# Kernel tuning notes

Measured on AMD Instinct MI355X. Metric: run time of the kernel, lower is better.

The kernel has to match this reference:

```python
import jax, jax.numpy as jnp
import numpy as np

N_NODES = 100000
N_EDGES = 1600000
D_NODE = 32
D_EDGE = 16
D_HID = 64
D_OUT = 32


def setup_inputs() -> dict:
    key = jax.random.key(0)
    ks = jax.random.split(key, 7)
    x = jax.random.normal(ks[0], (N_NODES, D_NODE), dtype=jnp.float32)
    edge_index = jax.random.randint(ks[1], (2, N_EDGES), 0, N_NODES, dtype=jnp.int64)
    edge_attr = jax.random.normal(ks[2], (N_EDGES, D_EDGE), dtype=jnp.float32)
    # 2-layer MLP params (Linear -> ReLU -> Linear), He-ish scaling
    W1 = jax.random.normal(ks[3], (D_NODE + D_EDGE, D_HID), dtype=jnp.float32) * (2.0 / (D_NODE + D_EDGE)) ** 0.5
    b1 = jnp.zeros((D_HID,), dtype=jnp.float32)
    W2 = jax.random.normal(ks[4], (D_HID, D_OUT), dtype=jnp.float32) * (2.0 / D_HID) ** 0.5
    b2 = jnp.zeros((D_OUT,), dtype=jnp.float32)
    return {"x": x, "edge_index": edge_index, "edge_attr": edge_attr,
            "W1": W1, "b1": b1, "W2": W2, "b2": b2}


def reference(x, edge_index, edge_attr, W1, b1, W2, b2):
    row, col = edge_index[0], edge_index[1]
    # gather source-node feats and concat with edge feats: [E, d_node + d_edge]
    inp = jnp.concatenate([x[col], edge_attr], axis=1)
    # 2-layer MLP over edges
    h = jax.nn.relu(inp @ W1 + b1)
    messages = h @ W2 + b2  # [E, d_out]
    # scatter-sum aggregate by destination node
    message = jax.ops.segment_sum(messages, row, num_segments=x.shape[0])
    return message
```

## Files before the change

kernel.cpp:

```cpp
#include <hip/hip_runtime.h>
#include <hip/hip_bf16.h>
#include <stdint.h>

#define N_NODES 100000
#define N_EDGES 1600000
#define D_NODE  32
#define D_EDGE  16
#define D_IN    48
#define D_HID   64
#define D_OUT   32

#define NBKT 98
#define BCAP 18432
#define SLICES (BCAP / 256)
#define S1_EDGES 2048
#define S1_NB 782
#define SCAN_NB 391

#define NFLAGS_OFF  ((size_t)0)
#define NB1_OFF     ((size_t)64)
#define NB2_OFF     ((size_t)320)
#define W1BF_OFF    ((size_t)1024)
#define W2BF_OFF    ((size_t)9216)
#define GCUR_OFF    ((size_t)16384)
#define XBF_OFF     ((size_t)65536)
#define TMPH_OFF    ((size_t)8388608)
#define TMPE_OFF    ((size_t)16777216)
#define REC_OFF     ((size_t)75497472)
#define ACCUM_OFF   ((size_t)90177536)

typedef __attribute__((ext_vector_type(8))) short bf16x8;
typedef __attribute__((ext_vector_type(4))) float f32x4;

__device__ inline float bf2f(unsigned int u16) {
    return __uint_as_float(u16 << 16);
}
__device__ inline unsigned short f2bf_rne(float f) {
    unsigned int x = __float_as_uint(f);
    unsigned int r = (x + 0x7FFFu + ((x >> 16) & 1u)) >> 16;
    return (unsigned short)r;
}
__device__ inline unsigned int pk_bf2(float a, float b) {
    float2 f; f.x = a; f.y = b;
    __hip_bfloat162 h = __float22bfloat162_rn(f);
    return *reinterpret_cast<unsigned int*>(&h);
}
__device__ inline float ld_f(const void* p, int i, int isbf) {
    if (isbf) return bf2f(((const unsigned short*)p)[i]);
    return ((const float*)p)[i];
}

__global__ __launch_bounds__(256) void prep_kernel(
        const void* __restrict__ xq, const void* __restrict__ idxq,
        const void* __restrict__ W1q, const void* __restrict__ b1q,
        const void* __restrict__ W2q, const void* __restrict__ b2q,
        char* __restrict__ ws) {
    const int t = threadIdx.x;
    const int i0 = blockIdx.x * 256 + t;

    __shared__ int s_isbf;
    if (t < 64) {
        unsigned short u = ((const unsigned short*)xq)[t];
        unsigned long long mb = __ballot(((u >> 7) & 0xFF) >= 140);
        if (t == 0) s_isbf = (mb == 0ULL);
    }

    float4* acc4 = (float4*)(ws + ACCUM_OFF);
    float4 z; z.x = z.y = z.z = z.w = 0.0f;
    for (int i = i0; i < (N_NODES + 1) * 32 / 4; i += SCAN_NB * 256) acc4[i] = z;

    __syncthreads();
    const int isbf = s_isbf;

    unsigned short* xbf = (unsigned short*)(ws + XBF_OFF);
    for (int i = i0; i < N_NODES * 32 / 8; i += SCAN_NB * 256) {
        uint4 o;
        if (isbf) {
            o = ((const uint4*)xq)[i];
        } else {
            const float4* xp = (const float4*)xq + i * 2;
            float4 a = xp[0], b = xp[1];
            o.x = pk_bf2(a.x, a.y); o.y = pk_bf2(a.z, a.w);
            o.z = pk_bf2(b.x, b.y); o.w = pk_bf2(b.z, b.w);
        }
        ((uint4*)xbf)[i] = o;
    }

    if (blockIdx.x != 0) return;

    if (t < NBKT) ((int*)(ws + GCUR_OFF))[t] = t * BCAP;
    if (t < 64) {
        int wodd = ((const int*)idxq)[2 * t + 1];
        unsigned long long mi = __ballot(wodd != 0);
        if (t == 0) {
            int* flags = (int*)(ws + NFLAGS_OFF);
            flags[0] = isbf;
            flags[1] = (mi == 0ULL);
        }
    }

    float* b1 = (float*)(ws + NB1_OFF);
    float* b2 = (float*)(ws + NB2_OFF);
    unsigned short* w1b = (unsigned short*)(ws + W1BF_OFF);
    unsigned short* w2b = (unsigned short*)(ws + W2BF_OFF);

    if (t < D_HID) b1[t] = ld_f(b1q, t, isbf);
    if (t < D_OUT) b2[t] = ld_f(b2q, t, isbf);

    for (int i = t; i < D_HID * 64; i += 256) {
        int n = i >> 6, k = i & 63;
        float v = (k < D_IN) ? ld_f(W1q, k * D_HID + n, isbf) : 0.0f;
        w1b[i] = f2bf_rne(v);
    }
    for (int i = t; i < D_OUT * 64; i += 256) {
        int n = i >> 6, k = i & 63;
        w2b[i] = f2bf_rne(ld_f(W2q, k * D_OUT + n, isbf));
    }
}

__global__ __launch_bounds__(256) void partition_kernel(
        const void* __restrict__ idxq, const void* __restrict__ eaq,
        char* __restrict__ ws) {
    const int is64 = ((const int*)(ws + NFLAGS_OFF))[1];
    const int isbf = ((const int*)(ws + NFLAGS_OFF))[0];
    __shared__ int hist[NBKT];
    __shared__ int base[NBKT];
    __shared__ int lcur[NBKT];
    const int t = threadIdx.x;
    if (t < NBKT) hist[t] = 0;
    __syncthreads();

    const int e0 = blockIdx.x * S1_EDGES;
    int dstv[8];
#pragma unroll
    for (int i = 0; i < 8; ++i) {
        const int e = e0 + i * 256 + t;
        int dst = -1;
        if (e < N_EDGES) {
            if (is64) dst = (int)((const long long*)idxq)[e];
            else      dst = ((const int*)idxq)[e];
            atomicAdd(&hist[dst >> 10], 1);
        }
        dstv[i] = dst;
    }
    __syncthreads();
    if (t < NBKT) {
        base[t] = atomicAdd((int*)(ws + GCUR_OFF) + t, hist[t]);
        lcur[t] = 0;
    }
    __syncthreads();

    unsigned int*   tmph = (unsigned int*)(ws + TMPH_OFF);
    unsigned short* tmpe = (unsigned short*)(ws + TMPE_OFF);
#pragma unroll
    for (int i = 0; i < 8; ++i) {
        const int e = e0 + i * 256 + t;
        if (e >= N_EDGES) continue;
        const int dst = dstv[i];
        int src;
        if (is64) src = (int)((const long long*)idxq)[N_EDGES + e];
        else      src = ((const int*)idxq)[N_EDGES + e];
        const int b = dst >> 10;
        const int r = atomicAdd(&lcur[b], 1);
        const size_t slot = (size_t)base[b] + r;

        tmph[slot] = (unsigned)src | ((unsigned)(dst & 1023) << 17);

        uint4 u;
        if (isbf) {
            const uint4* p = (const uint4*)((const unsigned short*)eaq + (size_t)e * 16);
            u = p[0];
            ((uint4*)(tmpe + slot * 16))[0] = u;
            u = p[1];
            ((uint4*)(tmpe + slot * 16))[1] = u;
        } else {
            const float4* p = (const float4*)((const float*)eaq + (size_t)e * 16);
            float4 a = p[0], b4 = p[1], c = p[2], d = p[3];
            u.x = pk_bf2(a.x, a.y);  u.y = pk_bf2(a.z, a.w);
            u.z = pk_bf2(b4.x, b4.y); u.w = pk_bf2(b4.z, b4.w);
            ((uint4*)(tmpe + slot * 16))[0] = u;
            u.x = pk_bf2(c.x, c.y);  u.y = pk_bf2(c.z, c.w);
            u.z = pk_bf2(d.x, d.y);  u.w = pk_bf2(d.z, d.w);
            ((uint4*)(tmpe + slot * 16))[1] = u;
        }
    }
}

__global__ __launch_bounds__(1024) void sort_kernel(char* __restrict__ ws) {
    __shared__ int hist[1024];
    __shared__ int cur[1024];
    const int b = blockIdx.x;
    const int t = threadIdx.x;
    hist[t] = 0;
    __syncthreads();

    const int cnt = ((const int*)(ws + GCUR_OFF))[b] - b * BCAP;
    const unsigned int* tmph = (const unsigned int*)(ws + TMPH_OFF) + (size_t)b * BCAP;
    unsigned long long* rec = (unsigned long long*)(ws + REC_OFF) + (size_t)b * BCAP;

    for (int i = t; i < cnt; i += 1024)
        atomicAdd(&hist[(tmph[i] >> 17) & 1023], 1);
    __syncthreads();

    int v = hist[t];
    for (int d = 1; d < 1024; d <<= 1) {
        int a = (t >= d) ? hist[t - d] : 0;
        __syncthreads();
        hist[t] += a;
        __syncthreads();
    }
    cur[t] = hist[t] - v;
    __syncthreads();

    for (int i = t; i < cnt; i += 1024) {
        unsigned int h = tmph[i];
        const int rd = (h >> 17) & 1023;
        const int rk = atomicAdd(&cur[rd], 1);
        unsigned long long out = ((unsigned long long)rd << 32)
                               | ((unsigned long long)(unsigned)i << 17)
                               | (h & 0x1FFFFu);
        rec[rk] = out;
    }
}

__global__ __launch_bounds__(256) void edge_mlp_agg_kernel(
        const char* __restrict__ wsro,
        float* __restrict__ accum) {
    const int b = blockIdx.y;
    const int cnt = ((const int*)(wsro + GCUR_OFF))[b] - b * BCAP;
    if (blockIdx.x * 256 >= cnt) return;

    __shared__ __align__(16) unsigned short hbuf[4][2][16][72];

    const int w   = threadIdx.x >> 6;
    const int l   = threadIdx.x & 63;
    const int m16 = l & 15;
    const int q   = l >> 4;

    const unsigned short* w1b = (const unsigned short*)(wsro + W1BF_OFF);
    const unsigned short* w2b = (const unsigned short*)(wsro + W2BF_OFF);
    const float* b1 = (const float*)(wsro + NB1_OFF);
    const float* b2 = (const float*)(wsro + NB2_OFF);
    const unsigned short* xbf  = (const unsigned short*)(wsro + XBF_OFF);
    const unsigned short* tmpe = (const unsigned short*)(wsro + TMPE_OFF) + (size_t)b * BCAP * 16;
    const unsigned long long* rec = (const unsigned long long*)(wsro + REC_OFF) + (size_t)b * BCAP;

    bf16x8 w1f[4][2], w2f[2][2];
#pragma unroll
    for (int t = 0; t < 4; ++t)
#pragma unroll
        for (int c = 0; c < 2; ++c)
            w1f[t][c] = *(const bf16x8*)(w1b + ((t * 16 + m16) * 64 + c * 32 + q * 8));
#pragma unroll
    for (int t = 0; t < 2; ++t)
#pragma unroll
        for (int c = 0; c < 2; ++c)
            w2f[t][c] = *(const bf16x8*)(w2b + ((t * 16 + m16) * 64 + c * 32 + q * 8));

    const int kb = blockIdx.x * 256 + w * 64;
    const int n0 = b << 10;

    int srcv[4], tixv[4], dstv[4];
#pragma unroll
    for (int g = 0; g < 4; ++g) {
        const int p = kb + g * 16 + m16;
        unsigned long long r = rec[p];
        if (p < cnt) {
            unsigned int lo = (unsigned int)r;
            srcv[g] = (int)(lo & 0x1FFFFu);
            tixv[g] = (int)(lo >> 17);
            dstv[g] = n0 + (int)(r >> 32);
        } else {
            srcv[g] = 0;
            tixv[g] = 0;
            dstv[g] = N_NODES;
        }
    }

    bf16x8 A0[4], A1[4];
#pragma unroll
    for (int g = 0; g < 4; ++g) {
        A0[g] = *(const bf16x8*)(xbf  + (size_t)srcv[g] * D_NODE + q * 8);
        A1[g] = *(const bf16x8*)(tmpe + (size_t)tixv[g] * 16 + (q & 1) * 8);
    }

    const float b1v[4] = { b1[m16], b1[16 + m16], b1[32 + m16], b1[48 + m16] };
    const float b2v[2] = { b2[m16], b2[16 + m16] };

    auto L1 = [&](int g, int bb) {
#pragma unroll
        for (int t = 0; t < 4; ++t) {
            f32x4 c;
            c[0] = c[1] = c[2] = c[3] = b1v[t];
            c = __builtin_amdgcn_mfma_f32_16x16x32_bf16(A0[g], w1f[t][0], c, 0, 0, 0);
            c = __builtin_amdgcn_mfma_f32_16x16x32_bf16(A1[g], w1f[t][1], c, 0, 0, 0);
            unsigned int u0 = pk_bf2(fmaxf(c[0], 0.0f), fmaxf(c[1], 0.0f));
            unsigned int u1 = pk_bf2(fmaxf(c[2], 0.0f), fmaxf(c[3], 0.0f));
            hbuf[w][bb][q * 4 + 0][t * 16 + m16] = (unsigned short)u0;
            hbuf[w][bb][q * 4 + 1][t * 16 + m16] = (unsigned short)(u0 >> 16);
            hbuf[w][bb][q * 4 + 2][t * 16 + m16] = (unsigned short)u1;
            hbuf[w][bb][q * 4 + 3][t * 16 + m16] = (unsigned short)(u1 >> 16);
        }
    };

    auto L2R = [&](int g, int bb) {
        bf16x8 a20 = *(const bf16x8*)(&hbuf[w][bb][m16][q * 8]);
        bf16x8 a21 = *(const bf16x8*)(&hbuf[w][bb][m16][32 + q * 8]);
        f32x4 c0, c1;
        c0[0] = c0[1] = c0[2] = c0[3] = b2v[0];
        c1[0] = c1[1] = c1[2] = c1[3] = b2v[1];
        c0 = __builtin_amdgcn_mfma_f32_16x16x32_bf16(a20, w2f[0][0], c0, 0, 0, 0);
        c0 = __builtin_amdgcn_mfma_f32_16x16x32_bf16(a21, w2f[0][1], c0, 0, 0, 0);
        c1 = __builtin_amdgcn_mfma_f32_16x16x32_bf16(a20, w2f[1][0], c1, 0, 0, 0);
        c1 = __builtin_amdgcn_mfma_f32_16x16x32_bf16(a21, w2f[1][1], c1, 0, 0, 0);

        const int dstw = dstv[g];
        int dprev = __shfl(dstw, (m16 + 15) & 15, 16);
        bool isStart = (m16 == 0) || (dprev != dstw);
        unsigned long long bal = __ballot(isStart);
        unsigned mask16 = (unsigned)(bal >> (l & 48)) & 0xFFFFu;
        int start = 0;
        while (start < 16) {
            unsigned rest = mask16 >> 1 >> start;
            int next = rest ? (start + 1 + (int)__builtin_ctz(rest)) : 16;
            int d = __shfl(dstw, start, 16);
            float s0 = 0.0f, s1 = 0.0f;
#pragma unroll
            for (int r = 0; r < 4; ++r) {
                int m = q * 4 + r;
                bool in = (m >= start) && (m < next);
                s0 += in ? c0[r] : 0.0f;
                s1 += in ? c1[r] : 0.0f;
            }
            s0 += __shfl_xor(s0, 16); s0 += __shfl_xor(s0, 32);
            s1 += __shfl_xor(s1, 16); s1 += __shfl_xor(s1, 32);
            if (q == 0) {
                unsafeAtomicAdd(accum + (size_t)d * 32 + m16,      s0);
                unsafeAtomicAdd(accum + (size_t)d * 32 + 16 + m16, s1);
            }
            start = next;
        }
    };

    L1(0, 0);
    L1(1, 1);
    L2R(0, 0);
    L1(2, 0);
    L2R(1, 1);
    L1(3, 1);
    L2R(2, 0);
    L2R(3, 1);
}

__global__ __launch_bounds__(256) void convert_kernel(
        const char* __restrict__ wsro, const float* __restrict__ accum,
        void* __restrict__ out) {
    const int isbf = ((const int*)(wsro + NFLAGS_OFF))[0];
    const int i = blockIdx.x * 256 + threadIdx.x;
    float4 v = ((const float4*)accum)[i];
    if (isbf) {
        uint2 u;
        u.x = pk_bf2(v.x, v.y);
        u.y = pk_bf2(v.z, v.w);
        ((uint2*)out)[i] = u;
    } else {
        ((float4*)out)[i] = v;
    }
}

extern "C" void kernel_launch(void* const* d_in, const int* in_sizes, int n_in,
                              void* d_out, int out_size, void* d_ws, size_t ws_size,
                              hipStream_t stream) {
    const void* x   = d_in[0];
    const void* idx = d_in[1];
    const void* ea  = d_in[2];
    const void* W1  = d_in[3];
    const void* b1  = d_in[4];
    const void* W2  = d_in[5];
    const void* b2  = d_in[6];
    char* ws = (char*)d_ws;

    hipLaunchKernelGGL(prep_kernel, dim3(SCAN_NB), dim3(256), 0, stream,
                       x, idx, W1, b1, W2, b2, ws);

    hipLaunchKernelGGL(partition_kernel, dim3(S1_NB), dim3(256), 0, stream, idx, ea, ws);

    hipLaunchKernelGGL(sort_kernel, dim3(NBKT), dim3(1024), 0, stream, ws);

    hipLaunchKernelGGL(edge_mlp_agg_kernel, dim3(SLICES, NBKT), dim3(256), 0, stream,
                       (const char*)ws, (float*)(ws + ACCUM_OFF));

    hipLaunchKernelGGL(convert_kernel, dim3(N_NODES * 32 / 4 / 256), dim3(256), 0, stream,
                       (const char*)ws, (const float*)(ws + ACCUM_OFF), d_out);
}
```

Measured before the change: 371.3 us.

## Stage partitioned edges in shared memory for coalesced bucket writes

The partition kernel now sorts each block's edges by bucket locally in LDS, using a prefix scan and padded payload arrays. It then writes headers and edge-attribute payloads to global memory in bucket-contiguous order, so the scattered stores become runs of contiguous addresses. Edges per block are halved to 1024 to fit the LDS staging buffers, which doubles the block count and the number of global atomic reservations. The extra scan and syncthreads add latency in exchange for better store coalescing.

```diff
diff --git a/kernel.cpp b/kernel.cpp
--- a/kernel.cpp
+++ b/kernel.cpp
@@ -13,8 +13,8 @@
 #define NBKT 98
 #define BCAP 18432
 #define SLICES (BCAP / 256)
-#define S1_EDGES 2048
-#define S1_NB 782
+#define S1_EDGES 1024
+#define S1_NB 1563
 #define SCAN_NB 391
 
 #define NFLAGS_OFF  ((size_t)0)
@@ -118,22 +118,31 @@
     }
 }
 
+#define PIDX(s) ((s) + ((s) >> 3))
 __global__ __launch_bounds__(256) void partition_kernel(
         const void* __restrict__ idxq, const void* __restrict__ eaq,
         char* __restrict__ ws) {
     const int is64 = ((const int*)(ws + NFLAGS_OFF))[1];
     const int isbf = ((const int*)(ws + NFLAGS_OFF))[0];
-    __shared__ int hist[NBKT];
-    __shared__ int base[NBKT];
-    __shared__ int lcur[NBKT];
+    __shared__ int hist[128];
+    __shared__ int sc[128];
+    __shared__ int lofs[128];
+    __shared__ int base[128];
+    __shared__ int lcur[128];
+    __shared__ unsigned int hdr[S1_EDGES];
+    __shared__ unsigned char bkt[S1_EDGES];
+    __shared__ __align__(16) uint4 pay[2][S1_EDGES + (S1_EDGES >> 3)];
+
     const int t = threadIdx.x;
-    if (t < NBKT) hist[t] = 0;
+    if (t < 128) hist[t] = 0;
     __syncthreads();
 
     const int e0 = blockIdx.x * S1_EDGES;
-    int dstv[8];
-#pragma unroll
-    for (int i = 0; i < 8; ++i) {
+    const int total = min(N_EDGES - e0, S1_EDGES);
+
+    int dstv[4];
+#pragma unroll
+    for (int i = 0; i < 4; ++i) {
         const int e = e0 + i * 256 + t;
         int dst = -1;
         if (e < N_EDGES) {
@@ -144,16 +153,25 @@
         dstv[i] = dst;
     }
     __syncthreads();
-    if (t < NBKT) {
-        base[t] = atomicAdd((int*)(ws + GCUR_OFF) + t, hist[t]);
+
+    if (t < 128) sc[t] = hist[t];
+    __syncthreads();
+    for (int d = 1; d < 128; d <<= 1) {
+        int a = 0;
+        if (t < 128 && t >= d) a = sc[t - d];
+        __syncthreads();
+        if (t < 128) sc[t] += a;
+        __syncthreads();
+    }
+    if (t < 128) {
+        lofs[t] = sc[t] - hist[t];
         lcur[t] = 0;
-    }
-    __syncthreads();
-
-    unsigned int*   tmph = (unsigned int*)(ws + TMPH_OFF);
-    unsigned short* tmpe = (unsigned short*)(ws + TMPE_OFF);
-#pragma unroll
-    for (int i = 0; i < 8; ++i) {
+        if (t < NBKT) base[t] = atomicAdd((int*)(ws + GCUR_OFF) + t, hist[t]);
+    }
+    __syncthreads();
+
+#pragma unroll
+    for (int i = 0; i < 4; ++i) {
         const int e = e0 + i * 256 + t;
         if (e >= N_EDGES) continue;
         const int dst = dstv[i];
@@ -162,27 +180,35 @@
         else      src = ((const int*)idxq)[N_EDGES + e];
         const int b = dst >> 10;
         const int r = atomicAdd(&lcur[b], 1);
-        const size_t slot = (size_t)base[b] + r;
-
-        tmph[slot] = (unsigned)src | ((unsigned)(dst & 1023) << 17);
-
-        uint4 u;
+        const int s = lofs[b] + r;
+        hdr[s] = (unsigned)src | ((unsigned)(dst & 1023) << 17);
+        bkt[s] = (unsigned char)b;
+
+        uint4 u0, u1;
         if (isbf) {
             const uint4* p = (const uint4*)((const unsigned short*)eaq + (size_t)e * 16);
-            u = p[0];
-            ((uint4*)(tmpe + slot * 16))[0] = u;
-            u = p[1];
-            ((uint4*)(tmpe + slot * 16))[1] = u;
+            u0 = p[0]; u1 = p[1];
         } else {
             const float4* p = (const float4*)((const float*)eaq + (size_t)e * 16);
             float4 a = p[0], b4 = p[1], c = p[2], d = p[3];
-            u.x = pk_bf2(a.x, a.y);  u.y = pk_bf2(a.z, a.w);
-            u.z = pk_bf2(b4.x, b4.y); u.w = pk_bf2(b4.z, b4.w);
-            ((uint4*)(tmpe + slot * 16))[0] = u;
-            u.x = pk_bf2(c.x, c.y);  u.y = pk_bf2(c.z, c.w);
-            u.z = pk_bf2(d.x, d.y);  u.w = pk_bf2(d.z, d.w);
-            ((uint4*)(tmpe + slot * 16))[1] = u;
-        }
+            u0.x = pk_bf2(a.x, a.y);  u0.y = pk_bf2(a.z, a.w);
+            u0.z = pk_bf2(b4.x, b4.y); u0.w = pk_bf2(b4.z, b4.w);
+            u1.x = pk_bf2(c.x, c.y);  u1.y = pk_bf2(c.z, c.w);
+            u1.z = pk_bf2(d.x, d.y);  u1.w = pk_bf2(d.z, d.w);
+        }
+        pay[0][PIDX(s)] = u0;
+        pay[1][PIDX(s)] = u1;
+    }
+    __syncthreads();
+
+    unsigned int* tmph = (unsigned int*)(ws + TMPH_OFF);
+    uint4*        tmp4 = (uint4*)(ws + TMPE_OFF);
+    for (int s = t; s < total; s += 256) {
+        const int b = bkt[s];
+        const size_t g = (size_t)base[b] + (s - lofs[b]);
+        tmph[g] = hdr[s];
+        tmp4[g * 2]     = pay[0][PIDX(s)];
+        tmp4[g * 2 + 1] = pay[1][PIDX(s)];
     }
 }
 
```

New measurement: 348.2 us. 1.07x faster.
